# Kernel tuning notes

Measured on AMD Instinct MI355X. Metric: run time of the kernel, lower is better.

Reference implementation:

```python
import jax, jax.numpy as jnp
import numpy as np

N = 8192
IN_F = 512
OUT_F = 128


def setup_inputs() -> dict:
    key = jax.random.key(0)
    k1, k2, k3, k4, k5, k6 = jax.random.split(key, 6)
    inp = jax.random.normal(k1, (N, IN_F), dtype=jnp.float32)
    adj = jax.random.randint(k2, (N, N), 0, 2).astype(jnp.float32)
    M = jax.random.uniform(k3, (N, N), dtype=jnp.float32)
    W = jax.random.normal(k4, (IN_F, OUT_F), dtype=jnp.float32) * (1.414 * np.sqrt(2.0 / (IN_F + OUT_F)))
    a_self = jax.random.normal(k5, (OUT_F, 1), dtype=jnp.float32) * (1.414 * np.sqrt(2.0 / (OUT_F + 1)))
    a_neighs = jax.random.normal(k6, (OUT_F, 1), dtype=jnp.float32) * (1.414 * np.sqrt(2.0 / (OUT_F + 1)))
    return {"input": inp, "adj": adj, "M": M, "W": W, "a_self": a_self, "a_neighs": a_neighs}


def reference(input, adj, M, W, a_self, a_neighs):
    h = input @ W                       # [N, OUT_F]
    attn_self = h @ a_self              # [N, 1]
    attn_neighs = h @ a_neighs          # [N, 1]
    e = attn_self + attn_neighs.T       # [N, N] broadcast add
    e = jax.nn.leaky_relu(e * M, negative_slope=0.2)
    e = jnp.where(adj > 0, e, jnp.float32(-9e15))
    attention = jax.nn.softmax(e, axis=1)
    h_prime = attention @ h             # [N, OUT_F]
    return jax.nn.elu(h_prime)          # concat=True
```

## Files before the change

kernel.cpp:

```cpp
#include <hip/hip_runtime.h>
#include <hip/hip_bf16.h>

typedef __attribute__((ext_vector_type(4))) float f32x4;
typedef __attribute__((ext_vector_type(8))) short s16x8;

constexpr int NN   = 8192;
constexpr int KIN  = 512;
constexpr int KOUT = 128;

constexpr int RBK  = 128;
constexpr int JC   = 4;
constexpr int JLEN = NN / JC;
constexpr int SGO  = 128;
constexpr int NS   = JLEN / SGO;
constexpr int SLAB = 128 * 256;

__device__ __forceinline__ ushort f2bf(float x) {
    union { float f; unsigned u; } v; v.f = x;
    unsigned r = (v.u + 0x7fffu + ((v.u >> 16) & 1u)) >> 16;
    return (ushort)r;
}

__device__ __forceinline__ void gload_lds16(const void* g, void* l) {
    __builtin_amdgcn_global_load_lds((const __attribute__((address_space(1))) void*)g,
                                     (__attribute__((address_space(3))) void*)l, 16, 0, 0);
}

__global__ __launch_bounds__(256) void kA(const float* __restrict__ inp,
                                          const float* __restrict__ W,
                                          const float* __restrict__ a_s,
                                          const float* __restrict__ a_n,
                                          ushort* __restrict__ hT,
                                          float* __restrict__ s_out,
                                          float* __restrict__ t_out) {
    __shared__ float smem[16 * 512];
    const int t = threadIdx.x;
    const int rbase = blockIdx.x * 16;

#pragma unroll
    for (int it = 0; it < 8; ++it) {
        int idx = it * 256 + t;
        int r = idx >> 7;
        int c4 = (idx & 127) << 2;
        *(f32x4*)(&smem[r * 512 + c4]) =
            *(const f32x4*)(inp + (size_t)(rbase + r) * KIN + c4);
    }
    __syncthreads();

    const int c0 = (t & 31) * 4;
    const int rg = (t >> 5) * 2;
    float acc[2][4] = {};
#pragma unroll 4
    for (int k = 0; k < KIN; ++k) {
        f32x4 w4 = *(const f32x4*)(W + (size_t)k * KOUT + c0);
        float a0 = smem[(rg + 0) * 512 + k];
        float a1 = smem[(rg + 1) * 512 + k];
#pragma unroll
        for (int cc = 0; cc < 4; ++cc) {
            acc[0][cc] += a0 * w4[cc];
            acc[1][cc] += a1 * w4[cc];
        }
    }
    __syncthreads();

    float* h_lds = smem;
#pragma unroll
    for (int rr = 0; rr < 2; ++rr) {
        f32x4 v = {acc[rr][0], acc[rr][1], acc[rr][2], acc[rr][3]};
        *(f32x4*)(&h_lds[(rg + rr) * 128 + c0]) = v;
    }
    __syncthreads();

    {
        const int col = t >> 1;
        const int r0 = (t & 1) * 8;
        ushort tmp[8];
#pragma unroll
        for (int rr = 0; rr < 8; ++rr) tmp[rr] = f2bf(h_lds[(r0 + rr) * 128 + col]);
        *(f32x4*)(hT + (size_t)col * NN + rbase + r0) = *(f32x4*)&tmp[0];
    }

    {
        const int w = t >> 6, lane = t & 63;
        float as1 = a_s[lane], as2 = a_s[64 + lane];
        float an1 = a_n[lane], an2 = a_n[64 + lane];
#pragma unroll
        for (int rr = 0; rr < 4; ++rr) {
            int row = w * 4 + rr;
            float h1 = h_lds[row * 128 + lane];
            float h2 = h_lds[row * 128 + 64 + lane];
            float ps = h1 * as1 + h2 * as2;
            float pt = h1 * an1 + h2 * an2;
#pragma unroll
            for (int off = 32; off; off >>= 1) {
                ps += __shfl_xor(ps, off);
                pt += __shfl_xor(pt, off);
            }
            if (lane == 0) {
                s_out[rbase + row] = ps;
                t_out[rbase + row] = pt;
            }
        }
    }
}

__global__ __launch_bounds__(512, 2) void kG(const float* __restrict__ Mmat,
                                             const float* __restrict__ adjm,
                                             const ushort* __restrict__ hT,
                                             const float* __restrict__ s_in,
                                             const float* __restrict__ t_in,
                                             float* __restrict__ o_part,
                                             float* __restrict__ l_part) {
    __shared__ __align__(16) char slab[2][SLAB];

    const int tid = threadIdx.x;
    const int w = tid >> 6;
    const int l = tid & 63;
    const int lrow = l & 15;
    const int kgrp = l >> 4;
    const int rb = blockIdx.x >> 2;
    const int jc = blockIdx.x & 3;
    const int j0 = jc * JLEN;
    const int row0 = rb * RBK;
    const int i = row0 + w * 16 + lrow;
    const int PH = rb & (NS - 1);

    const float si = s_in[i];

    const float* Mp = Mmat + (size_t)i * NN + j0 + kgrp * 8;
    const float* Ap = adjm + (size_t)i * NN + j0 + kgrp * 8;
    const float* tp = t_in + j0 + kgrp * 8;

    const ushort* hq[4];
#pragma unroll
    for (int q = 0; q < 4; ++q) {
        int r = w * 16 + q * 4 + (l >> 4);
        int sc = ((l & 15) ^ (r & 7)) * 8;
        hq[q] = hT + (size_t)r * NN + j0 + sc;
    }

    f32x4 acc[8];
#pragma unroll
    for (int ct = 0; ct < 8; ++ct) acc[ct] = (f32x4){0.f, 0.f, 0.f, 0.f};
    float lsum = 0.f;

    f32x4 gm0[4], gm1[4], ga0[4], ga1[4], gt0[4], gt1[4];

#define DMA_HT(P, SL)                                                            \
    _Pragma("unroll") for (int q = 0; q < 4; ++q)                                \
        gload_lds16(hq[q] + (P) * SGO, &slab[SL][0] + (w * 16 + q * 4) * 256);

#define LD_G(K, P)                                                               \
    {                                                                            \
        const float* mp_ = Mp + (P) * SGO + (K) * 32;                            \
        gm0[K] = *(const f32x4*)mp_;                                             \
        gm1[K] = *(const f32x4*)(mp_ + 4);                                       \
        const float* ap_ = Ap + (P) * SGO + (K) * 32;                            \
        ga0[K] = *(const f32x4*)ap_;                                             \
        ga1[K] = *(const f32x4*)(ap_ + 4);                                       \
        const float* tp_ = tp + (P) * SGO + (K) * 32;                            \
        gt0[K] = *(const f32x4*)tp_;                                             \
        gt1[K] = *(const f32x4*)(tp_ + 4);                                       \
    }

#define KSTEP(K, SL, PN)                                                         \
    {                                                                            \
        asm volatile("s_waitcnt vmcnt(22)" ::: "memory");                        \
        s16x8 af;                                                                \
        _Pragma("unroll")                                                        \
        for (int e = 0; e < 4; ++e) {                                            \
            float x = (si + gt0[K][e]) * gm0[K][e];                              \
            x = fmaxf(x, 0.2f * x);                                              \
            float p = __expf(x) * ga0[K][e];             \
            lsum += p;                                                           \
            af[e] = (short)f2bf(p);                                              \
        }                                                                        \
        _Pragma("unroll")                                                        \
        for (int e = 0; e < 4; ++e) {                                            \
            float x = (si + gt1[K][e]) * gm1[K][e];                              \
            x = fmaxf(x, 0.2f * x);                                              \
            float p = __expf(x) * ga1[K][e];                                     \
            lsum += p;                                                           \
            af[4 + e] = (short)f2bf(p);                                          \
        }                                                                        \
        const char* sb = &slab[SL][0];                                           \
        _Pragma("unroll")                                                        \
        for (int ct = 0; ct < 8; ++ct) {                                         \
            s16x8 bf = *(const s16x8*)(sb + (ct * 16 + lrow) * 256 +             \
                                       (((K) * 64 + kgrp * 16) ^ ((lrow & 7) << 4))); \
            acc[ct] = __builtin_amdgcn_mfma_f32_16x16x32_bf16(af, bf, acc[ct], 0, 0, 0); \
        }                                                                        \
        LD_G(K, PN)                                                              \
    }

    DMA_HT(PH, 0)
    LD_G(0, PH)
    LD_G(1, PH)
    LD_G(2, PH)
    LD_G(3, PH)
    asm volatile("s_waitcnt vmcnt(24)" ::: "memory");
    __builtin_amdgcn_s_barrier();
    asm volatile("" ::: "memory");

#pragma unroll 1
    for (int s = 0; s < NS; ++s) {
        const int pn = (s + 1 + PH) & (NS - 1);
        const int sl = s & 1;
        DMA_HT(pn, (s + 1) & 1)
        KSTEP(0, sl, pn)
        KSTEP(1, sl, pn)
        KSTEP(2, sl, pn)
        KSTEP(3, sl, pn)
        asm volatile("s_waitcnt vmcnt(24)" ::: "memory");
        __builtin_amdgcn_s_barrier();
        asm volatile("" ::: "memory");
    }
#undef DMA_HT
#undef LD_G
#undef KSTEP

    lsum += __shfl_xor(lsum, 16);
    lsum += __shfl_xor(lsum, 32);
    if (l < 16) l_part[(size_t)jc * NN + i] = lsum;

    float* op = o_part + (size_t)jc * NN * KOUT;
#pragma unroll
    for (int ct = 0; ct < 8; ++ct) {
#pragma unroll
        for (int r = 0; r < 4; ++r) {
            int gi = row0 + w * 16 + kgrp * 4 + r;
            int col = ct * 16 + lrow;
            op[(size_t)gi * KOUT + col] = acc[ct][r];
        }
    }
}

__global__ __launch_bounds__(256) void kC(const float* __restrict__ o_part,
                                          const float* __restrict__ l_part,
                                          float* __restrict__ out) {
    const int idx = blockIdx.x * 256 + threadIdx.x;
    const int i = idx >> 7;
    float osum = 0.f, lsum = 0.f;
#pragma unroll
    for (int p = 0; p < JC; ++p) {
        osum += o_part[(size_t)p * NN * KOUT + idx];
        lsum += l_part[(size_t)p * NN + i];
    }
    float v = osum / lsum;
    out[idx] = v > 0.f ? v : (__expf(v) - 1.f);
}

extern "C" void kernel_launch(void* const* d_in, const int* in_sizes, int n_in,
                              void* d_out, int out_size, void* d_ws, size_t ws_size,
                              hipStream_t stream) {
    const float* inp = (const float*)d_in[0];
    const float* adj = (const float*)d_in[1];
    const float* Mm  = (const float*)d_in[2];
    const float* W   = (const float*)d_in[3];
    const float* a_s = (const float*)d_in[4];
    const float* a_n = (const float*)d_in[5];
    float* out = (float*)d_out;

    char* ws = (char*)d_ws;
    ushort* hT    = (ushort*)(ws + 0);
    float*  s_buf = (float*)(ws + 2097152);
    float*  t_buf = (float*)(ws + 2129920);
    float*  l_prt = (float*)(ws + 2162688);
    float*  o_prt = (float*)(ws + 4194304);

    hipLaunchKernelGGL(kA, dim3(512), dim3(256), 0, stream, inp, W, a_s, a_n, hT, s_buf, t_buf);
    hipLaunchKernelGGL(kG, dim3(64 * JC), dim3(512), 0, stream, Mm, adj, hT, s_buf, t_buf, o_prt, l_prt);
    hipLaunchKernelGGL(kC, dim3(4096), dim3(256), 0, stream, o_prt, l_prt, out);
}
```

Before: 177.6 us.

## Load M/adj rows coalesced and stage bf16 probabilities through LDS for MFMA

Restructures the main attention kernel so each wave loads M and adj as contiguous 16-float row segments (four rows per wave instruction) rather than strided 8-float chunks. The computed probabilities are written to a per-wave LDS tile and read back in the MFMA A-operand layout. The stage width halves to 64 columns with smaller LDS slabs, and a full vmcnt(0) wait plus barrier now sits at the top of every iteration. The block phase offset is also rotated differently to spread accesses. This aims for better global coalescing at the cost of extra LDS traffic and a less overlapped pipeline with more frequent synchronization.

```diff
diff --git a/kernel.cpp b/kernel.cpp
--- a/kernel.cpp
+++ b/kernel.cpp
@@ -11,9 +11,10 @@
 constexpr int RBK  = 128;
 constexpr int JC   = 4;
 constexpr int JLEN = NN / JC;
-constexpr int SGO  = 128;
+constexpr int SGO  = 64;
 constexpr int NS   = JLEN / SGO;
-constexpr int SLAB = 128 * 256;
+constexpr int SLABSZ = 16384;
+constexpr int PBASE  = 32768;
 
 __device__ __forceinline__ ushort f2bf(float x) {
     union { float f; unsigned u; } v; v.f = x;
@@ -104,14 +105,14 @@
     }
 }
 
-__global__ __launch_bounds__(512, 2) void kG(const float* __restrict__ Mmat,
+__global__ __launch_bounds__(512, 1) void kH(const float* __restrict__ Mmat,
                                              const float* __restrict__ adjm,
                                              const ushort* __restrict__ hT,
                                              const float* __restrict__ s_in,
                                              const float* __restrict__ t_in,
                                              float* __restrict__ o_part,
                                              float* __restrict__ l_part) {
-    __shared__ __align__(16) char slab[2][SLAB];
+    __shared__ __align__(16) char LDS[49152];
 
     const int tid = threadIdx.x;
     const int w = tid >> 6;
@@ -122,106 +123,106 @@
     const int jc = blockIdx.x & 3;
     const int j0 = jc * JLEN;
     const int row0 = rb * RBK;
-    const int i = row0 + w * 16 + lrow;
-    const int PH = rb & (NS - 1);
-
-    const float si = s_in[i];
-
-    const float* Mp = Mmat + (size_t)i * NN + j0 + kgrp * 8;
-    const float* Ap = adjm + (size_t)i * NN + j0 + kgrp * 8;
-    const float* tp = t_in + j0 + kgrp * 8;
-
-    const ushort* hq[4];
-#pragma unroll
-    for (int q = 0; q < 4; ++q) {
-        int r = w * 16 + q * 4 + (l >> 4);
-        int sc = ((l & 15) ^ (r & 7)) * 8;
-        hq[q] = hT + (size_t)r * NN + j0 + sc;
+    const int PH = (int)((blockIdx.x * 5u) & (unsigned)(NS - 1));
+    const int POFF = PBASE + w * 2048;
+
+    float sreg[4];
+#pragma unroll
+    for (int q = 0; q < 4; ++q) sreg[q] = s_in[row0 + w * 16 + q * 4 + (l >> 4)];
+    float lsum4[4] = {0.f, 0.f, 0.f, 0.f};
+
+    const float* Mq = Mmat + (size_t)(row0 + w * 16 + (l >> 4)) * NN + j0 + (l & 15) * 4;
+    const float* Aq = adjm + (size_t)(row0 + w * 16 + (l >> 4)) * NN + j0 + (l & 15) * 4;
+    const float* tq = t_in + j0 + (l & 15) * 4;
+
+    const ushort* hq[2];
+#pragma unroll
+    for (int q2 = 0; q2 < 2; ++q2) {
+        int r = w * 16 + q2 * 8 + (l >> 3);
+        int sc = ((l & 7) ^ (r & 7)) * 8;
+        hq[q2] = hT + (size_t)r * NN + j0 + sc;
     }
 
     f32x4 acc[8];
 #pragma unroll
     for (int ct = 0; ct < 8; ++ct) acc[ct] = (f32x4){0.f, 0.f, 0.f, 0.f};
-    float lsum = 0.f;
-
-    f32x4 gm0[4], gm1[4], ga0[4], ga1[4], gt0[4], gt1[4];
+
+    f32x4 Mr[4], Ar[4], tr;
 
 #define DMA_HT(P, SL)                                                            \
-    _Pragma("unroll") for (int q = 0; q < 4; ++q)                                \
-        gload_lds16(hq[q] + (P) * SGO, &slab[SL][0] + (w * 16 + q * 4) * 256);
-
-#define LD_G(K, P)                                                               \
+    _Pragma("unroll") for (int q2 = 0; q2 < 2; ++q2)                             \
+        gload_lds16(hq[q2] + (size_t)(P) * SGO,                                  \
+                    LDS + (SL) * SLABSZ + (w * 16 + q2 * 8) * 128);
+
+#define LDG(P)                                                                   \
+    _Pragma("unroll") for (int q = 0; q < 4; ++q) {                              \
+        Mr[q] = *(const f32x4*)(Mq + (size_t)q * 4 * NN + (size_t)(P) * SGO);    \
+        Ar[q] = *(const f32x4*)(Aq + (size_t)q * 4 * NN + (size_t)(P) * SGO);    \
+    }                                                                            \
+    tr = *(const f32x4*)(tq + (size_t)(P) * SGO);
+
+#define EXPW_RELOAD(PN)                                                          \
     {                                                                            \
-        const float* mp_ = Mp + (P) * SGO + (K) * 32;                            \
-        gm0[K] = *(const f32x4*)mp_;                                             \
-        gm1[K] = *(const f32x4*)(mp_ + 4);                                       \
-        const float* ap_ = Ap + (P) * SGO + (K) * 32;                            \
-        ga0[K] = *(const f32x4*)ap_;                                             \
-        ga1[K] = *(const f32x4*)(ap_ + 4);                                       \
-        const float* tp_ = tp + (P) * SGO + (K) * 32;                            \
-        gt0[K] = *(const f32x4*)tp_;                                             \
-        gt1[K] = *(const f32x4*)(tp_ + 4);                                       \
-    }
-
-#define KSTEP(K, SL, PN)                                                         \
+        _Pragma("unroll") for (int q = 0; q < 4; ++q) {                          \
+            const int r = q * 4 + (l >> 4);                                      \
+            float pv[4];                                                         \
+            _Pragma("unroll") for (int e = 0; e < 4; ++e) {                      \
+                float x = (sreg[q] + tr[e]) * Mr[q][e];                          \
+                x = fmaxf(x, 0.2f * x);                                          \
+                float p = __expf(x) * Ar[q][e];          \
+                lsum4[q] += p;                                                   \
+                pv[e] = p;                                                       \
+            }                                                                    \
+            uint2 u;                                                             \
+            u.x = (unsigned)f2bf(pv[0]) | ((unsigned)f2bf(pv[1]) << 16);         \
+            u.y = (unsigned)f2bf(pv[2]) | ((unsigned)f2bf(pv[3]) << 16);         \
+            *(uint2*)(LDS + POFF + r * 128 + (((l & 15) * 8) ^ ((r & 7) << 4))) = u; \
+            Mr[q] = *(const f32x4*)(Mq + (size_t)q * 4 * NN + (size_t)(PN) * SGO);   \
+            Ar[q] = *(const f32x4*)(Aq + (size_t)q * 4 * NN + (size_t)(PN) * SGO);   \
+        }                                                                        \
+        tr = *(const f32x4*)(tq + (size_t)(PN) * SGO);                           \
+    }
+
+#define KSTEP(K, SL)                                                             \
     {                                                                            \
-        asm volatile("s_waitcnt vmcnt(22)" ::: "memory");                        \
-        s16x8 af;                                                                \
-        _Pragma("unroll")                                                        \
-        for (int e = 0; e < 4; ++e) {                                            \
-            float x = (si + gt0[K][e]) * gm0[K][e];                              \
-            x = fmaxf(x, 0.2f * x);                                              \
-            float p = __expf(x) * ga0[K][e];             \
-            lsum += p;                                                           \
-            af[e] = (short)f2bf(p);                                              \
-        }                                                                        \
-        _Pragma("unroll")                                                        \
-        for (int e = 0; e < 4; ++e) {                                            \
-            float x = (si + gt1[K][e]) * gm1[K][e];                              \
-            x = fmaxf(x, 0.2f * x);                                              \
-            float p = __expf(x) * ga1[K][e];                                     \
-            lsum += p;                                                           \
-            af[4 + e] = (short)f2bf(p);                                          \
-        }                                                                        \
-        const char* sb = &slab[SL][0];                                           \
-        _Pragma("unroll")                                                        \
-        for (int ct = 0; ct < 8; ++ct) {                                         \
-            s16x8 bf = *(const s16x8*)(sb + (ct * 16 + lrow) * 256 +             \
-                                       (((K) * 64 + kgrp * 16) ^ ((lrow & 7) << 4))); \
+        s16x8 af = *(const s16x8*)(LDS + POFF + lrow * 128 +                     \
+                                   ((((K) * 4 + kgrp) * 16) ^ ((lrow & 7) << 4))); \
+        _Pragma("unroll") for (int ct = 0; ct < 8; ++ct) {                       \
+            const int brow = ct * 16 + lrow;                                     \
+            s16x8 bf = *(const s16x8*)(LDS + (SL) * SLABSZ + brow * 128 +        \
+                                       ((((K) * 4 + kgrp) * 16) ^ ((lrow & 7) << 4))); \
             acc[ct] = __builtin_amdgcn_mfma_f32_16x16x32_bf16(af, bf, acc[ct], 0, 0, 0); \
         }                                                                        \
-        LD_G(K, PN)                                                              \
     }
 
     DMA_HT(PH, 0)
-    LD_G(0, PH)
-    LD_G(1, PH)
-    LD_G(2, PH)
-    LD_G(3, PH)
-    asm volatile("s_waitcnt vmcnt(24)" ::: "memory");
-    __builtin_amdgcn_s_barrier();
-    asm volatile("" ::: "memory");
+    LDG(PH)
 
 #pragma unroll 1
     for (int s = 0; s < NS; ++s) {
+        const int sl = s & 1;
         const int pn = (s + 1 + PH) & (NS - 1);
-        const int sl = s & 1;
-        DMA_HT(pn, (s + 1) & 1)
-        KSTEP(0, sl, pn)
-        KSTEP(1, sl, pn)
-        KSTEP(2, sl, pn)
-        KSTEP(3, sl, pn)
-        asm volatile("s_waitcnt vmcnt(24)" ::: "memory");
+        asm volatile("s_waitcnt vmcnt(0)" ::: "memory");
         __builtin_amdgcn_s_barrier();
         asm volatile("" ::: "memory");
+        DMA_HT(pn, sl ^ 1)
+        EXPW_RELOAD(pn)
+        KSTEP(0, sl)
+        KSTEP(1, sl)
     }
 #undef DMA_HT
-#undef LD_G
+#undef LDG
+#undef EXPW_RELOAD
 #undef KSTEP
 
-    lsum += __shfl_xor(lsum, 16);
-    lsum += __shfl_xor(lsum, 32);
-    if (l < 16) l_part[(size_t)jc * NN + i] = lsum;
+#pragma unroll
+    for (int q = 0; q < 4; ++q) {
+        float v = lsum4[q];
+#pragma unroll
+        for (int off = 1; off < 16; off <<= 1) v += __shfl_xor(v, off);
+        if ((l & 15) == 0)
+            l_part[(size_t)jc * NN + row0 + w * 16 + q * 4 + (l >> 4)] = v;
+    }
 
     float* op = o_part + (size_t)jc * NN * KOUT;
 #pragma unroll
@@ -269,6 +270,6 @@
     float*  o_prt = (float*)(ws + 4194304);
 
     hipLaunchKernelGGL(kA, dim3(512), dim3(256), 0, stream, inp, W, a_s, a_n, hT, s_buf, t_buf);
-    hipLaunchKernelGGL(kG, dim3(64 * JC), dim3(512), 0, stream, Mm, adj, hT, s_buf, t_buf, o_prt, l_prt);
+    hipLaunchKernelGGL(kH, dim3(64 * JC), dim3(512), 0, stream, Mm, adj, hT, s_buf, t_buf, o_prt, l_prt);
     hipLaunchKernelGGL(kC, dim3(4096), dim3(256), 0, stream, o_prt, l_prt, out);
 }
```

Result: slower. 206.2 us (+16.1%).
